# Performance work log

Hardware: AMD Instinct MI355X
Metric: run time of the kernel (lower is better)

Reference implementation:

```python
import jax, jax.numpy as jnp
import numpy as np

MUL = 32          # env_embed_multiplicity
E = 200000        # num edges
N = 12500         # num nodes
SQRT3 = 3.0 ** 0.5
AVG_NUM_NEIGH = 16.0


def _mlp2(x, W0, W1):
    # ScalarMLPFunction: linear layers with 1/sqrt(fan_in) normalization, SiLU between
    h = jax.nn.silu(x @ (W0 / jnp.sqrt(jnp.asarray(W0.shape[0], x.dtype))))
    return h @ (W1 / jnp.sqrt(jnp.asarray(W1.shape[0], x.dtype)))


def _env_weight(attr, w):
    # MakeWeightedChannels: per-edge, per-channel scalar weight for each irrep
    # attr: [E, 4] laid out as 1x0e (dim 1) + 1x1o (dim 3); w: [E, MUL*2]
    w = w.reshape(attr.shape[0], MUL, 2)
    idx = jnp.array([0, 1, 1, 1])  # irrep index of each component of attr
    return w[:, :, idx] * attr[:, None, :]  # [E, MUL, 4]


def setup_inputs() -> dict:
    key = jax.random.key(0)
    ks = jax.random.split(key, 16)
    rn = lambda k, s: jax.random.normal(k, s, dtype=jnp.float32)
    return {
        "edge_index": jax.random.randint(ks[0], (2, E), 0, N),
        "edge_attr": rn(ks[1], (E, 4)),
        "edge_invariants": jax.random.uniform(ks[2], (E, 8), dtype=jnp.float32),
        "W2b0": rn(ks[3], (8, 128)),
        "W2b1": rn(ks[4], (128, 128)),
        "Wenv0": rn(ks[5], (128, 128)),
        "Wlat1_0": rn(ks[6], (192, 128)),
        "Wlat1_1": rn(ks[7], (128, 128)),
        "Wenv1": rn(ks[8], (128, 64)),
        "Ws0": rn(ks[9], (64, 32)),
        "Wv0": rn(ks[10], (64, 32)),
        "Wfin0": rn(ks[11], (192, 128)),
        "Wfin1": rn(ks[12], (128, 128)),
        "num_nodes": N,
    }


def reference(edge_index, edge_attr, edge_invariants, W2b0, W2b1, Wenv0,
              Wlat1_0, Wlat1_1, Wenv1, Ws0, Wv0, Wfin0, Wfin1, num_nodes):
    center = edge_index[0]
    norm = 1.0 / jnp.sqrt(AVG_NUM_NEIGH)  # env_sum_normalizations = rsqrt(avg_num_neighbors)

    # ---- layer 0: two-body latent -> env weights (double numel at layer 0) ----
    lat = _mlp2(edge_invariants, W2b0, W2b1)                       # [E, 128]
    w = lat @ (Wenv0 / jnp.sqrt(128.0))                            # [E, 2*MUL*2]
    features = _env_weight(edge_attr, w[:, :2 * MUL])              # [E, MUL, 4]
    env_e = _env_weight(edge_attr, w[:, 2 * MUL:])                 # [E, MUL, 4]
    env = (jax.ops.segment_sum(env_e, center, num_segments=num_nodes) * norm)[center]

    # ---- layer 0 tensor product ('uuu', no weights), irreps 0e+1o ----
    x0, xv = features[:, :, 0], features[:, :, 1:]
    y0, yv = env[:, :, 0], env[:, :, 1:]
    out_ss = x0 * y0                                   # 0e x 0e -> 0e
    out_vv = jnp.sum(xv * yv, axis=-1) / SQRT3         # 1o x 1o -> 0e (w3j)
    out_sv = x0[:, :, None] * yv / SQRT3               # 0e x 1o -> 1o
    out_vs = xv * y0[:, :, None] / SQRT3               # 1o x 0e -> 1o
    scalars = jnp.stack([out_ss, out_vv], axis=-1).reshape(-1, 2 * MUL)

    # ---- layer 0 irreps-wise Linear: 2 paths -> 1 per irrep ----
    s_in = jnp.concatenate([out_ss, out_vv], axis=-1)              # [E, 2*MUL]
    s_out = s_in @ (Ws0 / jnp.sqrt(2.0 * MUL))                     # [E, MUL]
    v_in = jnp.concatenate([out_sv, out_vs], axis=1)               # [E, 2*MUL, 3]
    v_out = jnp.einsum('ecm,cd->edm', v_in, Wv0) / jnp.sqrt(2.0 * MUL)
    features = jnp.concatenate([s_out[:, :, None], v_out], axis=-1)  # [E, MUL, 4]

    # ---- layer 1 latent with resnet update ----
    new_lat = _mlp2(jnp.concatenate([lat, scalars], axis=-1), Wlat1_0, Wlat1_1)
    c = jnp.sqrt(0.5)  # resnet coeffs from zero-init log-params: cumsum [1,2,3]
    lat = c * lat + c * new_lat

    # ---- layer 1 env embedding + scatter ----
    w1 = lat @ (Wenv1 / jnp.sqrt(128.0))                           # [E, MUL*2]
    env_e1 = _env_weight(edge_attr, w1)
    env1 = (jax.ops.segment_sum(env_e1, center, num_segments=num_nodes) * norm)[center]

    # ---- layer 1 (last) tensor product: scalar outputs only ----
    s_ss = features[:, :, 0] * env1[:, :, 0]
    s_vv = jnp.sum(features[:, :, 1:] * env1[:, :, 1:], axis=-1) / SQRT3
    scalars1 = jnp.stack([s_ss, s_vv], axis=-1).reshape(-1, 2 * MUL)

    # ---- final latent + resnet ----
    new_lat = _mlp2(jnp.concatenate([lat, scalars1], axis=-1), Wfin0, Wfin1)
    out = jnp.sqrt(2.0 / 3.0) * lat + jnp.sqrt(1.0 / 3.0) * new_lat
    return out  # [E, 128] edge features (latent_out_field)
```

## Files before the change

kernel.cpp:

```cpp
#include <hip/hip_runtime.h>

typedef __attribute__((ext_vector_type(8))) short bf8_t;
typedef __attribute__((ext_vector_type(4))) short bf4_t;
typedef __attribute__((ext_vector_type(4))) float f4_t;
typedef unsigned short u16;
typedef unsigned int u32;

#define MFMA16 __builtin_amdgcn_mfma_f32_16x16x32_bf16

#define RSQRT8    0.35355339059327373f
#define RSQRT128  0.08838834764831845f
#define RSQRT192  0.07216878364870323f
#define RSQRT64   0.125f
#define INV_SQRT3 0.57735026918962576f
#define SEG_NORM  0.25f
#define C_HALF    0.70710678118654752f
#define SQ23      0.81649658092772603f
#define SQ13      0.57735026918962576f

__device__ __forceinline__ float bf2f(u16 b) {
    return __uint_as_float(((u32)b) << 16);
}
__device__ __forceinline__ u16 f2bf(float f) {
    u32 u = __float_as_uint(f);
    u += 0x7FFFu + ((u >> 16) & 1u);
    return (u16)(u >> 16);
}
__device__ __forceinline__ u32 cvtpk(float lo, float hi) {
    u32 r;
    asm("v_cvt_pk_bf16_f32 %0, %1, %2" : "=v"(r) : "v"(lo), "v"(hi));
    return r;
}
__device__ __forceinline__ u16 f2bf_hw(float f) { return (u16)cvtpk(f, f); }
__device__ __forceinline__ float silu_f(float x) {
    return x * __builtin_amdgcn_rcpf(1.0f + __expf(-x));
}

template<int KS, int NSTR, int AS>
__device__ __forceinline__ void gemm_rows(
    const u16* A,
    const u16* __restrict__ Wh, const u16* __restrict__ Wl,
    int lane, f4_t* acc)
{
    const int r = lane & 15;
    const int q = lane >> 4;
    const u16* ab = A + r * AS + q * 8;
    constexpr int CH = (KS > 4) ? 3 : KS;
#pragma unroll
    for (int c0 = 0; c0 < KS; c0 += CH) {
        bf8_t bh[CH], bl[CH];
#pragma unroll
        for (int j = 0; j < CH; ++j) {
            bh[j] = *(const bf8_t*)(Wh + ((c0 + j) * 64 + lane) * 8);
            bl[j] = *(const bf8_t*)(Wl + ((c0 + j) * 64 + lane) * 8);
        }
#pragma unroll
        for (int j = 0; j < CH; ++j) {
#pragma unroll
            for (int s = 0; s < NSTR; ++s) {
                bf8_t a = *(const bf8_t*)(ab + s * 16 * AS + (c0 + j) * 32);
                acc[s] = MFMA16(a, bl[j], acc[s], 0, 0, 0);
                acc[s] = MFMA16(a, bh[j], acc[s], 0, 0, 0);
            }
        }
    }
}

__device__ __forceinline__ void env_store(u16* dst, int w, float val, float4 av)
{
    int m = w >> 1;
    if ((w & 1) == 0) {
        dst[4 * m] = f2bf_hw(val * av.x);
    } else {
        dst[4 * m + 1] = f2bf_hw(val * av.y);
        *(u32*)(dst + 4 * m + 2) = cvtpk(val * av.z, val * av.w);
    }
}

struct PD { const float* src; u16* hi; u16* lo; int K, N, Kp, perm, off, cnt; };
struct PDs { PD d[10]; };

__global__ __launch_bounds__(256) void prep_all(PDs P, int total)
{
    int i = blockIdx.x * 256 + threadIdx.x;
    if (i >= total) return;
#pragma unroll
    for (int rg = 0; rg < 10; ++rg) {
        if (i >= P.d[rg].off && i < P.d[rg].off + P.d[rg].cnt) {
            int li = i - P.d[rg].off;
            int KS = P.d[rg].Kp >> 5;
            int tile = li / (KS * 512);
            int rem  = li - tile * KS * 512;
            int ks   = rem >> 9;
            int lane = (rem >> 3) & 63;
            int j    = rem & 7;
            int n = tile * 16 + (lane & 15);
            int k = ks * 32 + (lane >> 4) * 8 + j;
            int ksrc = k;
            if (P.d[rg].perm && k >= 128)
                ksrc = (k < 160) ? (128 + 2 * (k - 128)) : (129 + 2 * (k - 160));
            float wv = (ksrc < P.d[rg].K) ? P.d[rg].src[(size_t)ksrc * P.d[rg].N + n] : 0.f;
            u16 h = f2bf(wv);
            P.d[rg].hi[li] = h;
            P.d[rg].lo[li] = f2bf(wv - bf2f(h));
        }
    }
}

__global__ __launch_bounds__(256) void hist_k(const int* __restrict__ eidx,
                                              int* __restrict__ cnt, int E)
{
    int i = blockIdx.x * 256 + threadIdx.x;
    if (i < E) atomicAdd(&cnt[eidx[i]], 1);
}

__global__ __launch_bounds__(1024) void scan_k(const int* __restrict__ cnt,
                                               int* __restrict__ base,
                                               int* __restrict__ cursor, int NN)
{
    __shared__ int part[1024];
    const int t = threadIdx.x;
    const int CHK = (NN + 1023) >> 10;
    int s = 0;
    for (int k = 0; k < CHK; ++k) { int idx = t * CHK + k; if (idx < NN) s += cnt[idx]; }
    part[t] = s;
    __syncthreads();
    for (int off = 1; off < 1024; off <<= 1) {
        int v = (t >= off) ? part[t - off] : 0;
        __syncthreads();
        part[t] += v;
        __syncthreads();
    }
    if (t == 0) base[NN] = part[1023];
    int run = (t == 0) ? 0 : part[t - 1];
    for (int k = 0; k < CHK; ++k) {
        int idx = t * CHK + k;
        if (idx < NN) { base[idx] = run; cursor[idx] = run; run += cnt[idx]; }
    }
}

__global__ __launch_bounds__(256) void scatter_k(const int* __restrict__ eidx,
                                                 int* __restrict__ cursor,
                                                 int* __restrict__ sorted, int E)
{
    int i = blockIdx.x * 256 + threadIdx.x;
    if (i < E) {
        int p = atomicAdd(&cursor[eidx[i]], 1);
        sorted[p] = i;
    }
}

__global__ __launch_bounds__(256) void reduce_env(
    const int* __restrict__ base, const int* __restrict__ sorted,
    const u16* __restrict__ enve, u16* __restrict__ env, int NN)
{
    const int node = blockIdx.x * 4 + (threadIdx.x >> 6);
    const int ch = threadIdx.x & 63;
    if (node >= NN) return;
    const int b = base[node], en = base[node + 1];
    float a0 = 0.f, a1 = 0.f;
    int i = b;
    for (; i + 3 < en; i += 4) {
        int s0 = sorted[i], s1 = sorted[i + 1], s2 = sorted[i + 2], s3 = sorted[i + 3];
        u32 v0 = *(const u32*)(enve + (size_t)s0 * 128 + 2 * ch);
        u32 v1 = *(const u32*)(enve + (size_t)s1 * 128 + 2 * ch);
        u32 v2 = *(const u32*)(enve + (size_t)s2 * 128 + 2 * ch);
        u32 v3 = *(const u32*)(enve + (size_t)s3 * 128 + 2 * ch);
        a0 += (bf2f((u16)v0) + bf2f((u16)v1)) + (bf2f((u16)v2) + bf2f((u16)v3));
        a1 += (bf2f((u16)(v0 >> 16)) + bf2f((u16)(v1 >> 16))) + (bf2f((u16)(v2 >> 16)) + bf2f((u16)(v3 >> 16)));
    }
    for (; i < en; ++i) {
        u32 v = *(const u32*)(enve + (size_t)sorted[i] * 128 + 2 * ch);
        a0 += bf2f((u16)v);
        a1 += bf2f((u16)(v >> 16));
    }
    *(u32*)(env + (size_t)node * 128 + 2 * ch) = cvtpk(a0 * SEG_NORM, a1 * SEG_NORM);
}

__global__ __launch_bounds__(512, 6) void phaseA(
    const float* __restrict__ attr, const float* __restrict__ inv,
    const u16* __restrict__ Wh2b0, const u16* __restrict__ Wl2b0,
    const u16* __restrict__ Wh2b1, const u16* __restrict__ Wl2b1,
    const u16* __restrict__ Whenv0, const u16* __restrict__ Wlenv0,
    u16* __restrict__ latbuf, u16* __restrict__ featbuf,
    u16* __restrict__ enve, int E)
{
    __shared__ __align__(16) char sm[39936];
    u16 (*Xi)[32]  = (u16 (*)[32])sm;
    u16 (*Hs)[136] = (u16 (*)[136])(sm + 4096);
    u16 (*Ls)[136] = (u16 (*)[136])(sm + 21504);
    float (*sattr)[4] = (float (*)[4])(sm + 38912);

    const int tid = threadIdx.x;
    const int lane = tid & 63;
    const int w = tid >> 6;
    const int e0 = blockIdx.x * 64;
    const int E1 = E - 1;
    const int r = lane & 15, q = lane >> 4;
    const bool full = (e0 + 64 <= E);

    for (int i = tid; i < 64 * 32; i += 512) {
        int t = i >> 5, c = i & 31;
        u16 v = 0;
        if (c < 8) v = f2bf_hw(inv[(size_t)min(e0 + t, E1) * 8 + c]);
        Xi[t][c] = v;
    }
    if (tid < 256) { int t = tid >> 2, c = tid & 3; sattr[t][c] = attr[(size_t)min(e0 + t, E1) * 4 + c]; }
    __syncthreads();

    const f4_t z = {0.f, 0.f, 0.f, 0.f};
    f4_t acc[4];

#pragma unroll
    for (int s = 0; s < 4; ++s) acc[s] = z;
    gemm_rows<1, 4, 32>(&Xi[0][0], Wh2b0 + w * 512, Wl2b0 + w * 512, lane, acc);
#pragma unroll
    for (int s = 0; s < 4; ++s)
#pragma unroll
        for (int jj = 0; jj < 4; jj += 2) {
            u32 pk = cvtpk(silu_f(acc[s][jj] * RSQRT8), silu_f(acc[s][jj + 1] * RSQRT8));
            Hs[s * 16 + q * 4 + jj][w * 16 + r]     = (u16)pk;
            Hs[s * 16 + q * 4 + jj + 1][w * 16 + r] = (u16)(pk >> 16);
        }
    __syncthreads();

#pragma unroll
    for (int s = 0; s < 4; ++s) acc[s] = z;
    gemm_rows<4, 4, 136>(&Hs[0][0], Wh2b1 + w * 4 * 512, Wl2b1 + w * 4 * 512, lane, acc);
#pragma unroll
    for (int s = 0; s < 4; ++s)
#pragma unroll
        for (int jj = 0; jj < 4; jj += 2) {
            int row0 = s * 16 + q * 4 + jj, cc = w * 16 + r;
            u32 pk = cvtpk(acc[s][jj] * RSQRT128, acc[s][jj + 1] * RSQRT128);
            u16 b0 = (u16)pk, b1 = (u16)(pk >> 16);
            Ls[row0][cc] = b0;
            Ls[row0 + 1][cc] = b1;
            int ea = e0 + row0;
            if (full) {
                latbuf[(size_t)ea * 128 + cc] = b0;
                latbuf[(size_t)(ea + 1) * 128 + cc] = b1;
            } else {
                if (ea < E)     latbuf[(size_t)ea * 128 + cc] = b0;
                if (ea + 1 < E) latbuf[(size_t)(ea + 1) * 128 + cc] = b1;
            }
        }
    __syncthreads();

#pragma unroll
    for (int s = 0; s < 4; ++s) acc[s] = z;
    gemm_rows<4, 4, 136>(&Ls[0][0], Whenv0 + w * 4 * 512, Wlenv0 + w * 4 * 512, lane, acc);
    {
        const int col = w * 16 + r;
        u16* dstbase = (col < 64) ? featbuf : enve;
        const int wcol = col & 63;
        if (full) {
#pragma unroll
            for (int s = 0; s < 4; ++s)
#pragma unroll
                for (int jj = 0; jj < 4; ++jj) {
                    int row = s * 16 + q * 4 + jj;
                    float4 av = *(const float4*)&sattr[row][0];
                    env_store(dstbase + (size_t)(e0 + row) * 128, wcol, acc[s][jj] * RSQRT128, av);
                }
        } else {
#pragma unroll
            for (int s = 0; s < 4; ++s)
#pragma unroll
                for (int jj = 0; jj < 4; ++jj) {
                    int row = s * 16 + q * 4 + jj;
                    int e = e0 + row;
                    if (e >= E) continue;
                    float4 av = *(const float4*)&sattr[row][0];
                    env_store(dstbase + (size_t)e * 128, wcol, acc[s][jj] * RSQRT128, av);
                }
        }
    }
}

__global__ __launch_bounds__(512, 6) void phaseB(
    const int* __restrict__ eidx, const float* __restrict__ attr,
    const u16* __restrict__ env0b,
    const u16* __restrict__ Whs0, const u16* __restrict__ Wls0,
    const u16* __restrict__ Whv0, const u16* __restrict__ Wlv0,
    const u16* __restrict__ Whl10, const u16* __restrict__ Wll10,
    const u16* __restrict__ Whl11, const u16* __restrict__ Wll11,
    const u16* __restrict__ Whe1, const u16* __restrict__ Wle1,
    u16* __restrict__ latbuf, u16* __restrict__ featbuf,
    u16* __restrict__ enve, int E)
{
    __shared__ __align__(16) char sm[52480];
    u16 (*X4)[200] = (u16 (*)[200])sm;
    u16 (*P)[200]  = (u16 (*)[200])(sm + 25600);
    u16 (*Hs)[136] = (u16 (*)[136])(sm + 25600);
    float (*sattr)[4] = (float (*)[4])(sm + 51200);

    const int tid = threadIdx.x;
    const int lane = tid & 63;
    const int w = tid >> 6;
    const int e0 = blockIdx.x * 64;
    const int E1 = E - 1;
    const int r = lane & 15, q = lane >> 4;
    const bool full = (e0 + 64 <= E);

    if (tid < 256) { int t = tid >> 2, c = tid & 3; sattr[t][c] = attr[(size_t)min(e0 + t, E1) * 4 + c]; }

    for (int i = tid; i < 64 * 16; i += 512) {
        int t = i >> 4, dc = i & 15;
        *(bf8_t*)&X4[t][dc * 8] = ((const bf8_t*)(latbuf + (size_t)min(e0 + t, E1) * 128))[dc];
    }

    {
        const int t = tid >> 3, cg = tid & 7;
        const int e = min(e0 + t, E1);
        const int nd = eidx[e];
        const u16* fp = featbuf + (size_t)e * 128 + cg * 16;
        const u16* gp = env0b + (size_t)nd * 128 + cg * 16;
        bf8_t fA = *(const bf8_t*)fp;
        bf8_t fB = *(const bf8_t*)(fp + 8);
        bf8_t gA = *(const bf8_t*)gp;
        bf8_t gB = *(const bf8_t*)(gp + 8);
        float ssf[4], vvf[4], svf[3][4], vsf[3][4];
#pragma unroll
        for (int c = 0; c < 4; ++c) {
            float f0, f1, f2, f3, g0, g1, g2, g3;
            if (c < 2) {
                f0 = bf2f((u16)fA[4 * c]);     g0 = bf2f((u16)gA[4 * c]);
                f1 = bf2f((u16)fA[4 * c + 1]); g1 = bf2f((u16)gA[4 * c + 1]);
                f2 = bf2f((u16)fA[4 * c + 2]); g2 = bf2f((u16)gA[4 * c + 2]);
                f3 = bf2f((u16)fA[4 * c + 3]); g3 = bf2f((u16)gA[4 * c + 3]);
            } else {
                int cc = c - 2;
                f0 = bf2f((u16)fB[4 * cc]);     g0 = bf2f((u16)gB[4 * cc]);
                f1 = bf2f((u16)fB[4 * cc + 1]); g1 = bf2f((u16)gB[4 * cc + 1]);
                f2 = bf2f((u16)fB[4 * cc + 2]); g2 = bf2f((u16)gB[4 * cc + 2]);
                f3 = bf2f((u16)fB[4 * cc + 3]); g3 = bf2f((u16)gB[4 * cc + 3]);
            }
            ssf[c] = f0 * g0;
            vvf[c] = (f1 * g1 + f2 * g2 + f3 * g3) * INV_SQRT3;
            svf[0][c] = f0 * g1;  svf[1][c] = f0 * g2;  svf[2][c] = f0 * g3;
            vsf[0][c] = f1 * g0;  vsf[1][c] = f2 * g0;  vsf[2][c] = f3 * g0;
        }
        *(uint2*)&X4[t][128 + 4 * cg] = make_uint2(cvtpk(ssf[0], ssf[1]), cvtpk(ssf[2], ssf[3]));
        *(uint2*)&X4[t][160 + 4 * cg] = make_uint2(cvtpk(vvf[0], vvf[1]), cvtpk(vvf[2], vvf[3]));
#pragma unroll
        for (int d = 0; d < 3; ++d) {
            *(uint2*)&P[t][d * 64 + 4 * cg]      = make_uint2(cvtpk(svf[d][0], svf[d][1]), cvtpk(svf[d][2], svf[d][3]));
            *(uint2*)&P[t][d * 64 + 32 + 4 * cg] = make_uint2(cvtpk(vsf[d][0], vsf[d][1]), cvtpk(vsf[d][2], vsf[d][3]));
        }
    }
    __syncthreads();

    const f4_t z = {0.f, 0.f, 0.f, 0.f};

    {
        const int sw = w >> 1, cw = w & 1;
        f4_t aS = z, aV[3] = {z, z, z};
        const u16* bsh = Whs0 + cw * 2 * 512;
        const u16* bsl = Wls0 + cw * 2 * 512;
        const u16* bvh = Whv0 + cw * 2 * 512;
        const u16* bvl = Wlv0 + cw * 2 * 512;
        bf8_t s0h = *(const bf8_t*)(bsh + lane * 8);
        bf8_t s0l = *(const bf8_t*)(bsl + lane * 8);
        bf8_t s1h = *(const bf8_t*)(bsh + 512 + lane * 8);
        bf8_t s1l = *(const bf8_t*)(bsl + 512 + lane * 8);
        bf8_t v0h = *(const bf8_t*)(bvh + lane * 8);
        bf8_t v0l = *(const bf8_t*)(bvl + lane * 8);
        bf8_t v1h = *(const bf8_t*)(bvh + 512 + lane * 8);
        bf8_t v1l = *(const bf8_t*)(bvl + 512 + lane * 8);
        const u16* arow = &X4[sw * 16 + r][0];
        bf8_t a0 = *(const bf8_t*)(arow + 128 + q * 8);
        bf8_t a1 = *(const bf8_t*)(arow + 160 + q * 8);
        aS = MFMA16(a0, s0l, aS, 0, 0, 0);
        aS = MFMA16(a0, s0h, aS, 0, 0, 0);
        aS = MFMA16(a1, s1l, aS, 0, 0, 0);
        aS = MFMA16(a1, s1h, aS, 0, 0, 0);
        const u16* prow = &P[sw * 16 + r][0];
#pragma unroll
        for (int d = 0; d < 3; ++d) {
            bf8_t p0 = *(const bf8_t*)(prow + d * 64 + q * 8);
            bf8_t p1 = *(const bf8_t*)(prow + d * 64 + 32 + q * 8);
            aV[d] = MFMA16(p0, v0l, aV[d], 0, 0, 0);
            aV[d] = MFMA16(p0, v0h, aV[d], 0, 0, 0);
            aV[d] = MFMA16(p1, v1l, aV[d], 0, 0, 0);
            aV[d] = MFMA16(p1, v1h, aV[d], 0, 0, 0);
        }
        const int m = cw * 16 + r;
#pragma unroll
        for (int reg = 0; reg < 4; ++reg) {
            int e = e0 + sw * 16 + q * 4 + reg;
            if (full || e < E) {
                uint2 pv;
                pv.x = cvtpk(aS[reg] * RSQRT64,
                             aV[0][reg] * (RSQRT64 * INV_SQRT3));
                pv.y = cvtpk(aV[1][reg] * (RSQRT64 * INV_SQRT3),
                             aV[2][reg] * (RSQRT64 * INV_SQRT3));
                *(uint2*)(featbuf + (size_t)e * 128 + 4 * m) = pv;
            }
        }
    }

    f4_t acc[4];
#pragma unroll
    for (int s = 0; s < 4; ++s) acc[s] = z;
    gemm_rows<6, 4, 200>(&X4[0][0], Whl10 + w * 6 * 512, Wll10 + w * 6 * 512, lane, acc);
    __syncthreads();
#pragma unroll
    for (int s = 0; s < 4; ++s)
#pragma unroll
        for (int jj = 0; jj < 4; jj += 2) {
            u32 pk = cvtpk(silu_f(acc[s][jj] * RSQRT192), silu_f(acc[s][jj + 1] * RSQRT192));
            Hs[s * 16 + q * 4 + jj][w * 16 + r]     = (u16)pk;
            Hs[s * 16 + q * 4 + jj + 1][w * 16 + r] = (u16)(pk >> 16);
        }
    __syncthreads();

#pragma unroll
    for (int s = 0; s < 4; ++s) acc[s] = z;
    gemm_rows<4, 4, 136>(&Hs[0][0], Whl11 + w * 4 * 512, Wll11 + w * 4 * 512, lane, acc);
#pragma unroll
    for (int s = 0; s < 4; ++s)
#pragma unroll
        for (int jj = 0; jj < 4; jj += 2) {
            int row0 = s * 16 + q * 4 + jj, cc = w * 16 + r;
            float l2a = C_HALF * (bf2f(X4[row0][cc]) + acc[s][jj] * RSQRT128);
            float l2b = C_HALF * (bf2f(X4[row0 + 1][cc]) + acc[s][jj + 1] * RSQRT128);
            u32 pk = cvtpk(l2a, l2b);
            X4[row0][cc]     = (u16)pk;
            X4[row0 + 1][cc] = (u16)(pk >> 16);
        }
    __syncthreads();

    if (full) {
        for (int i = tid; i < 64 * 16; i += 512) {
            int t = i >> 4, dc = i & 15;
            ((bf8_t*)(latbuf + (size_t)(e0 + t) * 128))[dc] = *(const bf8_t*)&X4[t][dc * 8];
        }
    } else {
        for (int i = tid; i < 64 * 16; i += 512) {
            int t = i >> 4, dc = i & 15;
            int e = e0 + t;
            if (e < E) ((bf8_t*)(latbuf + (size_t)e * 128))[dc] = *(const bf8_t*)&X4[t][dc * 8];
        }
    }
    {
        const int ct = w & 3, rh = w >> 2;
        f4_t a6[2] = {z, z};
        gemm_rows<4, 2, 200>(&X4[rh * 32][0], Whe1 + ct * 4 * 512, Wle1 + ct * 4 * 512, lane, a6);
        const int col = ct * 16 + r;
#pragma unroll
        for (int s = 0; s < 2; ++s)
#pragma unroll
            for (int jj = 0; jj < 4; ++jj) {
                int row = rh * 32 + s * 16 + q * 4 + jj;
                int e = e0 + row;
                if (!full && e >= E) continue;
                float4 av = *(const float4*)&sattr[row][0];
                env_store(enve + (size_t)e * 128, col, a6[s][jj] * RSQRT128, av);
            }
    }
}

__global__ __launch_bounds__(512, 6) void phaseC(
    const int* __restrict__ eidx, const u16* __restrict__ env1b,
    const u16* __restrict__ Whf0, const u16* __restrict__ Wlf0,
    const u16* __restrict__ Whf1, const u16* __restrict__ Wlf1,
    const u16* __restrict__ latbuf, const u16* __restrict__ featbuf,
    float* __restrict__ outp, int E)
{
    __shared__ __align__(16) char sm[43008];
    u16 (*X7)[200] = (u16 (*)[200])sm;
    u16 (*Hs)[136] = (u16 (*)[136])(sm + 25600);

    const int tid = threadIdx.x;
    const int lane = tid & 63;
    const int w = tid >> 6;
    const int e0 = blockIdx.x * 64;
    const int E1 = E - 1;
    const int r = lane & 15, q = lane >> 4;
    const bool full = (e0 + 64 <= E);

    for (int i = tid; i < 64 * 16; i += 512) {
        int t = i >> 4, dc = i & 15;
        *(bf8_t*)&X7[t][dc * 8] = ((const bf8_t*)(latbuf + (size_t)min(e0 + t, E1) * 128))[dc];
    }

    {
        const int t = tid >> 3, cg = tid & 7;
        const int e = min(e0 + t, E1);
        const int nd = eidx[e];
        const u16* fp = featbuf + (size_t)e * 128 + cg * 16;
        const u16* gp = env1b + (size_t)nd * 128 + cg * 16;
        bf8_t fA = *(const bf8_t*)fp;
        bf8_t fB = *(const bf8_t*)(fp + 8);
        bf8_t gA = *(const bf8_t*)gp;
        bf8_t gB = *(const bf8_t*)(gp + 8);
        float ssf[4], vvf[4];
#pragma unroll
        for (int c = 0; c < 4; ++c) {
            float f0, f1, f2, f3, g0, g1, g2, g3;
            if (c < 2) {
                f0 = bf2f((u16)fA[4 * c]);     g0 = bf2f((u16)gA[4 * c]);
                f1 = bf2f((u16)fA[4 * c + 1]); g1 = bf2f((u16)gA[4 * c + 1]);
                f2 = bf2f((u16)fA[4 * c + 2]); g2 = bf2f((u16)gA[4 * c + 2]);
                f3 = bf2f((u16)fA[4 * c + 3]); g3 = bf2f((u16)gA[4 * c + 3]);
            } else {
                int cc = c - 2;
                f0 = bf2f((u16)fB[4 * cc]);     g0 = bf2f((u16)gB[4 * cc]);
                f1 = bf2f((u16)fB[4 * cc + 1]); g1 = bf2f((u16)gB[4 * cc + 1]);
                f2 = bf2f((u16)fB[4 * cc + 2]); g2 = bf2f((u16)gB[4 * cc + 2]);
                f3 = bf2f((u16)fB[4 * cc + 3]); g3 = bf2f((u16)gB[4 * cc + 3]);
            }
            ssf[c] = f0 * g0;
            vvf[c] = (f1 * g1 + f2 * g2 + f3 * g3) * INV_SQRT3;
        }
        *(uint2*)&X7[t][128 + 4 * cg] = make_uint2(cvtpk(ssf[0], ssf[1]), cvtpk(ssf[2], ssf[3]));
        *(uint2*)&X7[t][160 + 4 * cg] = make_uint2(cvtpk(vvf[0], vvf[1]), cvtpk(vvf[2], vvf[3]));
    }
    __syncthreads();

    const f4_t z = {0.f, 0.f, 0.f, 0.f};
    f4_t acc[4];
#pragma unroll
    for (int s = 0; s < 4; ++s) acc[s] = z;
    gemm_rows<6, 4, 200>(&X7[0][0], Whf0 + w * 6 * 512, Wlf0 + w * 6 * 512, lane, acc);
#pragma unroll
    for (int s = 0; s < 4; ++s)
#pragma unroll
        for (int jj = 0; jj < 4; jj += 2) {
            u32 pk = cvtpk(silu_f(acc[s][jj] * RSQRT192), silu_f(acc[s][jj + 1] * RSQRT192));
            Hs[s * 16 + q * 4 + jj][w * 16 + r]     = (u16)pk;
            Hs[s * 16 + q * 4 + jj + 1][w * 16 + r] = (u16)(pk >> 16);
        }
    __syncthreads();

#pragma unroll
    for (int s = 0; s < 4; ++s) acc[s] = z;
    gemm_rows<4, 4, 136>(&Hs[0][0], Whf1 + w * 4 * 512, Wlf1 + w * 4 * 512, lane, acc);
    if (full) {
#pragma unroll
        for (int s = 0; s < 4; ++s)
#pragma unroll
            for (int jj = 0; jj < 4; ++jj) {
                int row = s * 16 + q * 4 + jj, cc = w * 16 + r;
                outp[(size_t)(e0 + row) * 128 + cc] =
                    SQ23 * bf2f(X7[row][cc]) + SQ13 * (acc[s][jj] * RSQRT128);
            }
    } else {
#pragma unroll
        for (int s = 0; s < 4; ++s)
#pragma unroll
            for (int jj = 0; jj < 4; ++jj) {
                int row = s * 16 + q * 4 + jj, cc = w * 16 + r;
                int e = e0 + row;
                if (e < E)
                    outp[(size_t)e * 128 + cc] =
                        SQ23 * bf2f(X7[row][cc]) + SQ13 * (acc[s][jj] * RSQRT128);
            }
    }
}

extern "C" void kernel_launch(void* const* d_in, const int* in_sizes, int n_in,
                              void* d_out, int out_size, void* d_ws, size_t ws_size,
                              hipStream_t stream)
{
    const int E  = in_sizes[0] / 2;
    const int NN = 12500;

    const int*   eidx    = (const int*)d_in[0];
    const float* attr    = (const float*)d_in[1];
    const float* inv     = (const float*)d_in[2];
    float* outp = (float*)d_out;

    u16* latbuf  = (u16*)d_ws;
    u16* featbuf = latbuf + (size_t)E * 128;
    u16* env0b   = featbuf + (size_t)E * 128;
    u16* env1b   = env0b + (size_t)NN * 128;
    u16* p = env1b + (size_t)NN * 128;
    auto carve = [&](int elems) { u16* q0 = p; p += elems; return q0; };
    u16 *Wh2b0 = carve(128 * 32),  *Wl2b0 = carve(128 * 32);
    u16 *Wh2b1 = carve(128 * 128), *Wl2b1 = carve(128 * 128);
    u16 *Whe0  = carve(128 * 128), *Wle0  = carve(128 * 128);
    u16 *Whl10 = carve(128 * 192), *Wll10 = carve(128 * 192);
    u16 *Whl11 = carve(128 * 128), *Wll11 = carve(128 * 128);
    u16 *Whe1  = carve(64 * 128),  *Wle1  = carve(64 * 128);
    u16 *Whs0  = carve(32 * 64),   *Wls0  = carve(32 * 64);
    u16 *Whv0  = carve(32 * 64),   *Wlv0  = carve(32 * 64);
    u16 *Whf0  = carve(128 * 192), *Wlf0  = carve(128 * 192);
    u16 *Whf1  = carve(128 * 128), *Wlf1  = carve(128 * 128);
    int* cnt;
    {
        size_t off_bytes = (size_t)((char*)p - (char*)d_ws);
        off_bytes = (off_bytes + 3) & ~(size_t)3;
        cnt = (int*)((char*)d_ws + off_bytes);
    }
    int* base   = cnt + NN;
    int* cursor = base + NN + 1;
    int* sorted = cursor + NN;

    u16* enve = (u16*)d_out;

    hipMemsetAsync(cnt, 0, NN * sizeof(int), stream);

    PDs P;
    auto setpd = [&](int i, const float* s, u16* h, u16* l, int K, int N, int Kp, int pm, int off) {
        P.d[i] = {s, h, l, K, N, Kp, pm, off, N * Kp};
    };
    setpd(0, (const float*)d_in[3],  Wh2b0, Wl2b0,   8, 128,  32, 0, 0);
    setpd(1, (const float*)d_in[4],  Wh2b1, Wl2b1, 128, 128, 128, 0, 4096);
    setpd(2, (const float*)d_in[5],  Whe0,  Wle0,  128, 128, 128, 0, 20480);
    setpd(3, (const float*)d_in[6],  Whl10, Wll10, 192, 128, 192, 1, 36864);
    setpd(4, (const float*)d_in[7],  Whl11, Wll11, 128, 128, 128, 0, 61440);
    setpd(5, (const float*)d_in[8],  Whe1,  Wle1,  128,  64, 128, 0, 77824);
    setpd(6, (const float*)d_in[9],  Whs0,  Wls0,   64,  32,  64, 0, 86016);
    setpd(7, (const float*)d_in[10], Whv0,  Wlv0,   64,  32,  64, 0, 88064);
    setpd(8, (const float*)d_in[11], Whf0,  Wlf0,  192, 128, 192, 1, 90112);
    setpd(9, (const float*)d_in[12], Whf1,  Wlf1,  128, 128, 128, 0, 114688);
    const int total = 131072;
    prep_all<<<(total + 255) / 256, 256, 0, stream>>>(P, total);

    hist_k<<<(E + 255) / 256, 256, 0, stream>>>(eidx, cnt, E);
    scan_k<<<1, 1024, 0, stream>>>(cnt, base, cursor, NN);
    scatter_k<<<(E + 255) / 256, 256, 0, stream>>>(eidx, cursor, sorted, E);

    const int nb = (E + 63) / 64;
    phaseA<<<nb, 512, 0, stream>>>(attr, inv, Wh2b0, Wl2b0, Wh2b1, Wl2b1,
                                   Whe0, Wle0, latbuf, featbuf, enve, E);
    reduce_env<<<(NN + 3) / 4, 256, 0, stream>>>(base, sorted, enve, env0b, NN);
    phaseB<<<nb, 512, 0, stream>>>(eidx, attr, env0b, Whs0, Wls0, Whv0, Wlv0,
                                   Whl10, Wll10, Whl11, Wll11, Whe1, Wle1,
                                   latbuf, featbuf, enve, E);
    reduce_env<<<(NN + 3) / 4, 256, 0, stream>>>(base, sorted, enve, env1b, NN);
    phaseC<<<nb, 512, 0, stream>>>(eidx, env1b, Whf0, Wlf0, Whf1, Wlf1,
                                   latbuf, featbuf, outp, E);
}
```

Baseline: 409.8 us.

## Store raw env weights per edge and expand with attrs inside consumers

PhaseA and phaseB now write compact per-edge channel weights (64 bf16 per edge) instead of the expanded [MUL,4] env/feature tensors (128 bf16). reduce_env and phaseB multiply by edge_attr on the fly when they read these buffers. The goal is to halve the intermediate write and gather traffic and drop the shared-memory attr staging. The histogram kernel is also merged into the weight-prep kernel to save a launch. In exchange, reduce_env does extra gathers of attr rows and some redundant multiplies.

```diff
diff --git a/kernel.cpp b/kernel.cpp
--- a/kernel.cpp
+++ b/kernel.cpp
@@ -66,23 +66,15 @@
     }
 }
 
-__device__ __forceinline__ void env_store(u16* dst, int w, float val, float4 av)
-{
-    int m = w >> 1;
-    if ((w & 1) == 0) {
-        dst[4 * m] = f2bf_hw(val * av.x);
-    } else {
-        dst[4 * m + 1] = f2bf_hw(val * av.y);
-        *(u32*)(dst + 4 * m + 2) = cvtpk(val * av.z, val * av.w);
-    }
-}
-
 struct PD { const float* src; u16* hi; u16* lo; int K, N, Kp, perm, off, cnt; };
 struct PDs { PD d[10]; };
 
-__global__ __launch_bounds__(256) void prep_all(PDs P, int total)
+__global__ __launch_bounds__(256) void prep_all(PDs P, int total,
+                                                const int* __restrict__ eidx,
+                                                int* __restrict__ cnt, int E)
 {
     int i = blockIdx.x * 256 + threadIdx.x;
+    if (i < E) atomicAdd(&cnt[eidx[i]], 1);
     if (i >= total) return;
 #pragma unroll
     for (int rg = 0; rg < 10; ++rg) {
@@ -107,13 +99,6 @@
     }
 }
 
-__global__ __launch_bounds__(256) void hist_k(const int* __restrict__ eidx,
-                                              int* __restrict__ cnt, int E)
-{
-    int i = blockIdx.x * 256 + threadIdx.x;
-    if (i < E) atomicAdd(&cnt[eidx[i]], 1);
-}
-
 __global__ __launch_bounds__(1024) void scan_k(const int* __restrict__ cnt,
                                                int* __restrict__ base,
                                                int* __restrict__ cursor, int NN)
@@ -152,44 +137,57 @@
 
 __global__ __launch_bounds__(256) void reduce_env(
     const int* __restrict__ base, const int* __restrict__ sorted,
-    const u16* __restrict__ enve, u16* __restrict__ env, int NN)
+    const u16* __restrict__ envw, const float* __restrict__ attr,
+    u16* __restrict__ env, int NN)
 {
     const int node = blockIdx.x * 4 + (threadIdx.x >> 6);
     const int ch = threadIdx.x & 63;
     if (node >= NN) return;
     const int b = base[node], en = base[node + 1];
+    const int wo = ch & ~1;
+    const int ao = (ch & 1) * 2;
+    const bool odd = (ch & 1) != 0;
     float a0 = 0.f, a1 = 0.f;
     int i = b;
     for (; i + 3 < en; i += 4) {
         int s0 = sorted[i], s1 = sorted[i + 1], s2 = sorted[i + 2], s3 = sorted[i + 3];
-        u32 v0 = *(const u32*)(enve + (size_t)s0 * 128 + 2 * ch);
-        u32 v1 = *(const u32*)(enve + (size_t)s1 * 128 + 2 * ch);
-        u32 v2 = *(const u32*)(enve + (size_t)s2 * 128 + 2 * ch);
-        u32 v3 = *(const u32*)(enve + (size_t)s3 * 128 + 2 * ch);
-        a0 += (bf2f((u16)v0) + bf2f((u16)v1)) + (bf2f((u16)v2) + bf2f((u16)v3));
-        a1 += (bf2f((u16)(v0 >> 16)) + bf2f((u16)(v1 >> 16))) + (bf2f((u16)(v2 >> 16)) + bf2f((u16)(v3 >> 16)));
+        u32 w0 = *(const u32*)(envw + (size_t)s0 * 64 + wo);
+        u32 w1 = *(const u32*)(envw + (size_t)s1 * 64 + wo);
+        u32 w2 = *(const u32*)(envw + (size_t)s2 * 64 + wo);
+        u32 w3 = *(const u32*)(envw + (size_t)s3 * 64 + wo);
+        float2 v0 = *(const float2*)(attr + (size_t)s0 * 4 + ao);
+        float2 v1 = *(const float2*)(attr + (size_t)s1 * 4 + ao);
+        float2 v2 = *(const float2*)(attr + (size_t)s2 * 4 + ao);
+        float2 v3 = *(const float2*)(attr + (size_t)s3 * 4 + ao);
+        float l0 = bf2f((u16)(odd ? (w0 >> 16) : w0)), h0 = bf2f((u16)(w0 >> 16));
+        float l1 = bf2f((u16)(odd ? (w1 >> 16) : w1)), h1 = bf2f((u16)(w1 >> 16));
+        float l2 = bf2f((u16)(odd ? (w2 >> 16) : w2)), h2 = bf2f((u16)(w2 >> 16));
+        float l3 = bf2f((u16)(odd ? (w3 >> 16) : w3)), h3 = bf2f((u16)(w3 >> 16));
+        a0 += (l0 * v0.x + l1 * v1.x) + (l2 * v2.x + l3 * v3.x);
+        a1 += (h0 * v0.y + h1 * v1.y) + (h2 * v2.y + h3 * v3.y);
     }
     for (; i < en; ++i) {
-        u32 v = *(const u32*)(enve + (size_t)sorted[i] * 128 + 2 * ch);
-        a0 += bf2f((u16)v);
-        a1 += bf2f((u16)(v >> 16));
+        int s0 = sorted[i];
+        u32 w0 = *(const u32*)(envw + (size_t)s0 * 64 + wo);
+        float2 v0 = *(const float2*)(attr + (size_t)s0 * 4 + ao);
+        a0 += bf2f((u16)(odd ? (w0 >> 16) : w0)) * v0.x;
+        a1 += bf2f((u16)(w0 >> 16)) * v0.y;
     }
     *(u32*)(env + (size_t)node * 128 + 2 * ch) = cvtpk(a0 * SEG_NORM, a1 * SEG_NORM);
 }
 
 __global__ __launch_bounds__(512, 6) void phaseA(
-    const float* __restrict__ attr, const float* __restrict__ inv,
+    const float* __restrict__ inv,
     const u16* __restrict__ Wh2b0, const u16* __restrict__ Wl2b0,
     const u16* __restrict__ Wh2b1, const u16* __restrict__ Wl2b1,
     const u16* __restrict__ Whenv0, const u16* __restrict__ Wlenv0,
-    u16* __restrict__ latbuf, u16* __restrict__ featbuf,
-    u16* __restrict__ enve, int E)
-{
-    __shared__ __align__(16) char sm[39936];
+    u16* __restrict__ latbuf, u16* __restrict__ featw,
+    u16* __restrict__ envw, int E)
+{
+    __shared__ __align__(16) char sm[38912];
     u16 (*Xi)[32]  = (u16 (*)[32])sm;
     u16 (*Hs)[136] = (u16 (*)[136])(sm + 4096);
     u16 (*Ls)[136] = (u16 (*)[136])(sm + 21504);
-    float (*sattr)[4] = (float (*)[4])(sm + 38912);
 
     const int tid = threadIdx.x;
     const int lane = tid & 63;
@@ -205,7 +203,6 @@
         if (c < 8) v = f2bf_hw(inv[(size_t)min(e0 + t, E1) * 8 + c]);
         Xi[t][c] = v;
     }
-    if (tid < 256) { int t = tid >> 2, c = tid & 3; sattr[t][c] = attr[(size_t)min(e0 + t, E1) * 4 + c]; }
     __syncthreads();
 
     const f4_t z = {0.f, 0.f, 0.f, 0.f};
@@ -252,48 +249,41 @@
     gemm_rows<4, 4, 136>(&Ls[0][0], Whenv0 + w * 4 * 512, Wlenv0 + w * 4 * 512, lane, acc);
     {
         const int col = w * 16 + r;
-        u16* dstbase = (col < 64) ? featbuf : enve;
+        u16* dstbase = (col < 64) ? featw : envw;
         const int wcol = col & 63;
-        if (full) {
-#pragma unroll
-            for (int s = 0; s < 4; ++s)
-#pragma unroll
-                for (int jj = 0; jj < 4; ++jj) {
-                    int row = s * 16 + q * 4 + jj;
-                    float4 av = *(const float4*)&sattr[row][0];
-                    env_store(dstbase + (size_t)(e0 + row) * 128, wcol, acc[s][jj] * RSQRT128, av);
+#pragma unroll
+        for (int s = 0; s < 4; ++s)
+#pragma unroll
+            for (int jj = 0; jj < 4; jj += 2) {
+                int row0 = s * 16 + q * 4 + jj;
+                u32 pk = cvtpk(acc[s][jj] * RSQRT128, acc[s][jj + 1] * RSQRT128);
+                int ea = e0 + row0;
+                if (full) {
+                    dstbase[(size_t)ea * 64 + wcol] = (u16)pk;
+                    dstbase[(size_t)(ea + 1) * 64 + wcol] = (u16)(pk >> 16);
+                } else {
+                    if (ea < E)     dstbase[(size_t)ea * 64 + wcol] = (u16)pk;
+                    if (ea + 1 < E) dstbase[(size_t)(ea + 1) * 64 + wcol] = (u16)(pk >> 16);
                 }
-        } else {
-#pragma unroll
-            for (int s = 0; s < 4; ++s)
-#pragma unroll
-                for (int jj = 0; jj < 4; ++jj) {
-                    int row = s * 16 + q * 4 + jj;
-                    int e = e0 + row;
-                    if (e >= E) continue;
-                    float4 av = *(const float4*)&sattr[row][0];
-                    env_store(dstbase + (size_t)e * 128, wcol, acc[s][jj] * RSQRT128, av);
-                }
-        }
+            }
     }
 }
 
 __global__ __launch_bounds__(512, 6) void phaseB(
     const int* __restrict__ eidx, const float* __restrict__ attr,
     const u16* __restrict__ env0b,
+    const u16* __restrict__ featw, u16* __restrict__ envw,
     const u16* __restrict__ Whs0, const u16* __restrict__ Wls0,
     const u16* __restrict__ Whv0, const u16* __restrict__ Wlv0,
     const u16* __restrict__ Whl10, const u16* __restrict__ Wll10,
     const u16* __restrict__ Whl11, const u16* __restrict__ Wll11,
     const u16* __restrict__ Whe1, const u16* __restrict__ Wle1,
-    u16* __restrict__ latbuf, u16* __restrict__ featbuf,
-    u16* __restrict__ enve, int E)
-{
-    __shared__ __align__(16) char sm[52480];
+    u16* __restrict__ latbuf, u16* __restrict__ featbuf, int E)
+{
+    __shared__ __align__(16) char sm[51200];
     u16 (*X4)[200] = (u16 (*)[200])sm;
     u16 (*P)[200]  = (u16 (*)[200])(sm + 25600);
     u16 (*Hs)[136] = (u16 (*)[136])(sm + 25600);
-    float (*sattr)[4] = (float (*)[4])(sm + 51200);
 
     const int tid = threadIdx.x;
     const int lane = tid & 63;
@@ -303,8 +293,6 @@
     const int r = lane & 15, q = lane >> 4;
     const bool full = (e0 + 64 <= E);
 
-    if (tid < 256) { int t = tid >> 2, c = tid & 3; sattr[t][c] = attr[(size_t)min(e0 + t, E1) * 4 + c]; }
-
     for (int i = tid; i < 64 * 16; i += 512) {
         int t = i >> 4, dc = i & 15;
         *(bf8_t*)&X4[t][dc * 8] = ((const bf8_t*)(latbuf + (size_t)min(e0 + t, E1) * 128))[dc];
@@ -314,27 +302,25 @@
         const int t = tid >> 3, cg = tid & 7;
         const int e = min(e0 + t, E1);
         const int nd = eidx[e];
-        const u16* fp = featbuf + (size_t)e * 128 + cg * 16;
+        bf8_t wv = *(const bf8_t*)(featw + (size_t)e * 64 + cg * 8);
         const u16* gp = env0b + (size_t)nd * 128 + cg * 16;
-        bf8_t fA = *(const bf8_t*)fp;
-        bf8_t fB = *(const bf8_t*)(fp + 8);
         bf8_t gA = *(const bf8_t*)gp;
         bf8_t gB = *(const bf8_t*)(gp + 8);
+        float4 av = *(const float4*)(attr + (size_t)e * 4);
         float ssf[4], vvf[4], svf[3][4], vsf[3][4];
 #pragma unroll
         for (int c = 0; c < 4; ++c) {
-            float f0, f1, f2, f3, g0, g1, g2, g3;
+            float wf0 = bf2f((u16)wv[2 * c]);
+            float wf1 = bf2f((u16)wv[2 * c + 1]);
+            float f0 = wf0 * av.x, f1 = wf1 * av.y, f2 = wf1 * av.z, f3 = wf1 * av.w;
+            float g0, g1, g2, g3;
             if (c < 2) {
-                f0 = bf2f((u16)fA[4 * c]);     g0 = bf2f((u16)gA[4 * c]);
-                f1 = bf2f((u16)fA[4 * c + 1]); g1 = bf2f((u16)gA[4 * c + 1]);
-                f2 = bf2f((u16)fA[4 * c + 2]); g2 = bf2f((u16)gA[4 * c + 2]);
-                f3 = bf2f((u16)fA[4 * c + 3]); g3 = bf2f((u16)gA[4 * c + 3]);
+                g0 = bf2f((u16)gA[4 * c]);     g1 = bf2f((u16)gA[4 * c + 1]);
+                g2 = bf2f((u16)gA[4 * c + 2]); g3 = bf2f((u16)gA[4 * c + 3]);
             } else {
                 int cc = c - 2;
-                f0 = bf2f((u16)fB[4 * cc]);     g0 = bf2f((u16)gB[4 * cc]);
-                f1 = bf2f((u16)fB[4 * cc + 1]); g1 = bf2f((u16)gB[4 * cc + 1]);
-                f2 = bf2f((u16)fB[4 * cc + 2]); g2 = bf2f((u16)gB[4 * cc + 2]);
-                f3 = bf2f((u16)fB[4 * cc + 3]); g3 = bf2f((u16)gB[4 * cc + 3]);
+                g0 = bf2f((u16)gB[4 * cc]);     g1 = bf2f((u16)gB[4 * cc + 1]);
+                g2 = bf2f((u16)gB[4 * cc + 2]); g3 = bf2f((u16)gB[4 * cc + 3]);
             }
             ssf[c] = f0 * g0;
             vvf[c] = (f1 * g1 + f2 * g2 + f3 * g3) * INV_SQRT3;
@@ -451,12 +437,17 @@
 #pragma unroll
         for (int s = 0; s < 2; ++s)
 #pragma unroll
-            for (int jj = 0; jj < 4; ++jj) {
-                int row = rh * 32 + s * 16 + q * 4 + jj;
-                int e = e0 + row;
-                if (!full && e >= E) continue;
-                float4 av = *(const float4*)&sattr[row][0];
-                env_store(enve + (size_t)e * 128, col, a6[s][jj] * RSQRT128, av);
+            for (int jj = 0; jj < 4; jj += 2) {
+                int row0 = rh * 32 + s * 16 + q * 4 + jj;
+                u32 pk = cvtpk(a6[s][jj] * RSQRT128, a6[s][jj + 1] * RSQRT128);
+                int ea = e0 + row0;
+                if (full) {
+                    envw[(size_t)ea * 64 + col] = (u16)pk;
+                    envw[(size_t)(ea + 1) * 64 + col] = (u16)(pk >> 16);
+                } else {
+                    if (ea < E)     envw[(size_t)ea * 64 + col] = (u16)pk;
+                    if (ea + 1 < E) envw[(size_t)(ea + 1) * 64 + col] = (u16)(pk >> 16);
+                }
             }
     }
 }
@@ -598,7 +589,8 @@
     int* cursor = base + NN + 1;
     int* sorted = cursor + NN;
 
-    u16* enve = (u16*)d_out;
+    u16* featw = (u16*)d_out;
+    u16* envw  = featw + (size_t)E * 64;
 
     hipMemsetAsync(cnt, 0, NN * sizeof(int), stream);
 
@@ -617,20 +609,21 @@
     setpd(8, (const float*)d_in[11], Whf0,  Wlf0,  192, 128, 192, 1, 90112);
     setpd(9, (const float*)d_in[12], Whf1,  Wlf1,  128, 128, 128, 0, 114688);
     const int total = 131072;
-    prep_all<<<(total + 255) / 256, 256, 0, stream>>>(P, total);
-
-    hist_k<<<(E + 255) / 256, 256, 0, stream>>>(eidx, cnt, E);
+    const int span = (E > total) ? E : total;
+    prep_all<<<(span + 255) / 256, 256, 0, stream>>>(P, total, eidx, cnt, E);
+
     scan_k<<<1, 1024, 0, stream>>>(cnt, base, cursor, NN);
     scatter_k<<<(E + 255) / 256, 256, 0, stream>>>(eidx, cursor, sorted, E);
 
     const int nb = (E + 63) / 64;
-    phaseA<<<nb, 512, 0, stream>>>(attr, inv, Wh2b0, Wl2b0, Wh2b1, Wl2b1,
-                                   Whe0, Wle0, latbuf, featbuf, enve, E);
-    reduce_env<<<(NN + 3) / 4, 256, 0, stream>>>(base, sorted, enve, env0b, NN);
-    phaseB<<<nb, 512, 0, stream>>>(eidx, attr, env0b, Whs0, Wls0, Whv0, Wlv0,
+    phaseA<<<nb, 512, 0, stream>>>(inv, Wh2b0, Wl2b0, Wh2b1, Wl2b1,
+                                   Whe0, Wle0, latbuf, featw, envw, E);
+    reduce_env<<<(NN + 3) / 4, 256, 0, stream>>>(base, sorted, envw, attr, env0b, NN);
+    phaseB<<<nb, 512, 0, stream>>>(eidx, attr, env0b, featw, envw,
+                                   Whs0, Wls0, Whv0, Wlv0,
                                    Whl10, Wll10, Whl11, Wll11, Whe1, Wle1,
-                                   latbuf, featbuf, enve, E);
-    reduce_env<<<(NN + 3) / 4, 256, 0, stream>>>(base, sorted, enve, env1b, NN);
+                                   latbuf, featbuf, E);
+    reduce_env<<<(NN + 3) / 4, 256, 0, stream>>>(base, sorted, envw, attr, env1b, NN);
     phaseC<<<nb, 512, 0, stream>>>(eidx, env1b, Whf0, Wlf0, Whf1, Wlf1,
                                    latbuf, featbuf, outp, E);
 }
```

After: 374.0 us. 1.1x faster.
